# Kernel tuning notes

Hardware: AMD Instinct MI355X
Metric: run time of the kernel (lower is better)

## Reference

```python
import jax, jax.numpy as jnp
import numpy as np

D = 1024      # hidden_size
H = 16        # num_attention_heads
HD = D // H   # head_dim
FF = 4096     # intermediate_size
EPS = 1e-5

def layernorm(x, g, b):
    mu = jnp.mean(x, axis=-1, keepdims=True)
    var = jnp.mean(jnp.square(x - mu), axis=-1, keepdims=True)
    return (x - mu) * jax.lax.rsqrt(var + EPS) * g + b

def setup_inputs() -> dict:
    key = jax.random.key(0)
    ks = jax.random.split(key, 16)
    s = 0.02
    return {
        "x":   jax.random.normal(ks[0], (4, 1024, D), jnp.float32),
        "wq":  jax.random.normal(ks[1], (D, D), jnp.float32) * s,
        "bq":  jnp.zeros((D,), jnp.float32),
        "wk":  jax.random.normal(ks[2], (D, D), jnp.float32) * s,
        "bk":  jnp.zeros((D,), jnp.float32),
        "wv":  jax.random.normal(ks[3], (D, D), jnp.float32) * s,
        "bv":  jnp.zeros((D,), jnp.float32),
        "wo":  jax.random.normal(ks[4], (D, D), jnp.float32) * s,
        "bo":  jnp.zeros((D,), jnp.float32),
        "w1":  jax.random.normal(ks[5], (D, FF), jnp.float32) * s,
        "b1":  jnp.zeros((FF,), jnp.float32),
        "w2":  jax.random.normal(ks[6], (FF, D), jnp.float32) * s,
        "b2":  jnp.zeros((D,), jnp.float32),
        "ln1_g": jnp.ones((D,), jnp.float32),
        "ln1_b": jnp.zeros((D,), jnp.float32),
        "ln2_g": jnp.ones((D,), jnp.float32),
        "ln2_b": jnp.zeros((D,), jnp.float32),
    }

def reference(x, wq, bq, wk, bk, wv, bv, wo, bo, w1, b1, w2, b2,
              ln1_g, ln1_b, ln2_g, ln2_b):
    B, S, _ = x.shape
    # --- pre-LN multi-head attention (per-head linears fused as one GEMM) ---
    h = layernorm(x, ln1_g, ln1_b)
    q = (h @ wq + bq).reshape(B, S, H, HD).transpose(0, 2, 1, 3)  # [B,H,S,hd]
    k = (h @ wk + bk).reshape(B, S, H, HD).transpose(0, 2, 1, 3)
    v = (h @ wv + bv).reshape(B, S, H, HD).transpose(0, 2, 1, 3)
    scores = jnp.einsum('bhqd,bhkd->bhqk', q, k) / np.sqrt(HD).astype(x.dtype)
    weights = jax.nn.softmax(scores, axis=-1)  # dropout p=0 -> identity
    attn = jnp.einsum('bhqk,bhkd->bhqd', weights, v)
    attn = attn.transpose(0, 2, 1, 3).reshape(B, S, D)
    x = x + attn @ wo + bo
    # --- pre-LN feed-forward with exact GELU ---
    h2 = layernorm(x, ln2_g, ln2_b)
    ffn = jax.nn.gelu(h2 @ w1 + b1, approximate=False) @ w2 + b2
    return x + ffn
```

## Files before the change

kernel.cpp:

```cpp
#include <hip/hip_runtime.h>
#include <hip/hip_bf16.h>
#include <cstdint>

#define S_LEN  1024
#define DMODEL 1024
#define NTOK   4096
#define NHEAD  16
#define HDIM   64
#define FFDIM  4096
#define NBATCH 4
#define QSCALE 0.1803368801f

using bf16x8 = __attribute__((ext_vector_type(8))) short;
using f32x4  = __attribute__((ext_vector_type(4))) float;

__device__ __forceinline__ ushort f2bf(float f) {
  union { float f; uint32_t u; } a; a.f = f;
  uint32_t u = a.u;
  u += 0x7FFFu + ((u >> 16) & 1u);
  return (ushort)(u >> 16);
}
__device__ __forceinline__ ushort f2bf_hw(float f) {
  uint32_t r;
  asm("v_cvt_pk_bf16_f32 %0, %1, %1" : "=v"(r) : "v"(f));
  return (ushort)r;
}
__device__ __forceinline__ float bf2f(ushort u) {
  union { uint32_t u; float f; } c; c.u = ((uint32_t)u) << 16; return c.f;
}
__device__ __forceinline__ float ld_as_float(const float* p, long i) { return p[i]; }
__device__ __forceinline__ float ld_as_float(const ushort* p, long i) { return bf2f(p[i]); }
__device__ __forceinline__ void st_out(float* C, long i, float v) { C[i] = v; }
__device__ __forceinline__ void st_out(ushort* C, long i, float v) { C[i] = f2bf(v); }

__device__ __forceinline__ void gld_lds16(const void* g, void* l) {
  __builtin_amdgcn_global_load_lds((const __attribute__((address_space(1))) void*)g,
                                   (__attribute__((address_space(3))) void*)l, 16, 0, 0);
}

__global__ __launch_bounds__(256) void ln_kernel(const float* __restrict__ x,
    const float* __restrict__ g, const float* __restrict__ b,
    ushort* __restrict__ out) {
  int row = blockIdx.x;
  int tid = threadIdx.x;
  const float4* xr = (const float4*)(x + (long)row * DMODEL);
  float4 v = xr[tid];
  float s  = v.x + v.y + v.z + v.w;
  float s2 = v.x*v.x + v.y*v.y + v.z*v.z + v.w*v.w;
  for (int off = 32; off; off >>= 1) { s += __shfl_down(s, off); s2 += __shfl_down(s2, off); }
  __shared__ float red[8];
  int wid = tid >> 6, lane = tid & 63;
  if (lane == 0) { red[wid] = s; red[wid + 4] = s2; }
  __syncthreads();
  if (tid == 0) {
    red[0] = red[0] + red[1] + red[2] + red[3];
    red[4] = red[4] + red[5] + red[6] + red[7];
  }
  __syncthreads();
  float mu  = red[0] * (1.0f / DMODEL);
  float var = red[4] * (1.0f / DMODEL) - mu * mu;
  float rs  = rsqrtf(var + 1e-5f);
  float4 gg = ((const float4*)g)[tid];
  float4 bb = ((const float4*)b)[tid];
  ushort4 o;
  o.x = f2bf((v.x - mu) * rs * gg.x + bb.x);
  o.y = f2bf((v.y - mu) * rs * gg.y + bb.y);
  o.z = f2bf((v.z - mu) * rs * gg.z + bb.z);
  o.w = f2bf((v.w - mu) * rs * gg.w + bb.w);
  ((ushort4*)(out + (long)row * DMODEL))[tid] = o;
}

__global__ __launch_bounds__(256) void concat3(const float* __restrict__ a,
    const float* __restrict__ b, const float* __restrict__ c, float* __restrict__ o) {
  int i = blockIdx.x * 256 + threadIdx.x;
  o[i] = (i < 1024) ? a[i] : ((i < 2048) ? b[i - 1024] : c[i - 2048]);
}

template <int NP>
__global__ __launch_bounds__(256) void reduce_add(
    const ushort* __restrict__ parts, const float* __restrict__ bias,
    float* __restrict__ out) {
  long i = (long)blockIdx.x * 256 + threadIdx.x;
  const long PSTRIDE = (long)NTOK * DMODEL / 4;
  float4 acc = ((const float4*)out)[i];
  float4 b = ((const float4*)bias)[i & 255];
  acc.x += b.x; acc.y += b.y; acc.z += b.z; acc.w += b.w;
#pragma unroll
  for (int z = 0; z < NP; ++z) {
    ushort4 u = ((const ushort4*)parts)[z * PSTRIDE + i];
    acc.x += bf2f(u.x); acc.y += bf2f(u.y); acc.z += bf2f(u.z); acc.w += bf2f(u.w);
  }
  ((float4*)out)[i] = acc;
}

template <int NP>
__global__ __launch_bounds__(256) void reduce_ln(
    const ushort* __restrict__ parts, const float* __restrict__ xres,
    const float* __restrict__ bias, float* __restrict__ out,
    const float* __restrict__ g, const float* __restrict__ bln,
    ushort* __restrict__ hout) {
  int row = blockIdx.x, tid = threadIdx.x;
  long i = (long)row * 256 + tid;
  const long PSTRIDE = (long)NTOK * DMODEL / 4;
  float4 v = ((const float4*)xres)[i];
  float4 b = ((const float4*)bias)[tid];
  v.x += b.x; v.y += b.y; v.z += b.z; v.w += b.w;
#pragma unroll
  for (int z = 0; z < NP; ++z) {
    ushort4 u = ((const ushort4*)parts)[z * PSTRIDE + i];
    v.x += bf2f(u.x); v.y += bf2f(u.y); v.z += bf2f(u.z); v.w += bf2f(u.w);
  }
  ((float4*)out)[i] = v;
  float s  = v.x + v.y + v.z + v.w;
  float s2 = v.x*v.x + v.y*v.y + v.z*v.z + v.w*v.w;
  for (int off = 32; off; off >>= 1) { s += __shfl_down(s, off); s2 += __shfl_down(s2, off); }
  __shared__ float red[8];
  int wid = tid >> 6, lane = tid & 63;
  if (lane == 0) { red[wid] = s; red[wid + 4] = s2; }
  __syncthreads();
  if (tid == 0) {
    red[0] = red[0] + red[1] + red[2] + red[3];
    red[4] = red[4] + red[5] + red[6] + red[7];
  }
  __syncthreads();
  float mu  = red[0] * (1.0f / DMODEL);
  float var = red[4] * (1.0f / DMODEL) - mu * mu;
  float rs  = rsqrtf(var + 1e-5f);
  float4 gg = ((const float4*)g)[tid];
  float4 bb = ((const float4*)bln)[tid];
  ushort4 o;
  o.x = f2bf((v.x - mu) * rs * gg.x + bb.x);
  o.y = f2bf((v.y - mu) * rs * gg.y + bb.y);
  o.z = f2bf((v.z - mu) * rs * gg.z + bb.z);
  o.w = f2bf((v.w - mu) * rs * gg.w + bb.w);
  ((ushort4*)hout)[i] = o;
}

template <typename TIN>
__global__ __launch_bounds__(256) void transpose_cvt(const TIN* __restrict__ in,
    ushort* __restrict__ out, int ldin, int ldout,
    long inZhi, long inZlo, long outZ) {
  int z = blockIdx.z;
  in  += (long)(z >> 4) * inZhi + (long)(z & 15) * inZlo;
  out += (long)z * outZ;
  __shared__ float tile[32][33];
  int c0 = blockIdx.x * 32, r0 = blockIdx.y * 32;
  int tx = threadIdx.x, ty = threadIdx.y;
  for (int i = ty; i < 32; i += 8)
    tile[i][tx] = ld_as_float(in, (long)(r0 + i) * ldin + c0 + tx);
  __syncthreads();
  for (int i = ty; i < 32; i += 8)
    out[(long)(c0 + i) * ldout + r0 + tx] = f2bf(tile[tx][i]);
}

template <int ACT, bool BIAS, bool RES, typename TOUT>
__global__ __launch_bounds__(256) void gemm_bt(
    const ushort* __restrict__ A, const ushort* __restrict__ BT, TOUT* __restrict__ C,
    const float* __restrict__ bias, const float* __restrict__ resp,
    int M, int K, int lda, int ldb, int ldc,
    long aZhi, long aZlo, long bZhi, long bZlo, long cZhi, long cZlo) {
  __shared__ __align__(16) ushort lA[2][128 * 64];
  __shared__ __align__(16) ushort lB[2][128 * 64];
  int z = blockIdx.z;
  A  += (long)(z >> 4) * aZhi + (long)(z & 15) * aZlo;
  BT += (long)(z >> 4) * bZhi + (long)(z & 15) * bZlo;
  long coff = (long)(z >> 4) * cZhi + (long)(z & 15) * cZlo;
  int gx = gridDim.x;
  int nwg = gx * gridDim.y;
  int lin = blockIdx.x + gx * blockIdx.y;
  int wg = (lin & 7) * (nwg >> 3) + (lin >> 3);
  int n0 = (wg / gx) * 128, m0 = (wg % gx) * 128;
  int tid = threadIdx.x, lane = tid & 63, wid = tid >> 6;
  int wr = wid >> 1, wc = wid & 1;
  int lrow = lane >> 3;
  int swz = ((lane & 7) ^ lrow) << 3;
  int Mm1 = M - 1;
  f32x4 acc[4][4];
#pragma unroll
  for (int i = 0; i < 4; i++)
#pragma unroll
    for (int j = 0; j < 4; j++) acc[i][j] = (f32x4){0.f, 0.f, 0.f, 0.f};

  auto STAGE = [&](int kt, int buf) {
    const ushort* Ak = A + (kt << 6) + swz;
    const ushort* Bk = BT + (kt << 6) + swz;
#pragma unroll
    for (int c = 0; c < 4; ++c) {
      int ch = (wid << 2) | c;
      int rb = (ch << 3) + lrow;
      gld_lds16(Ak + (long)(n0 + rb) * lda, &lA[buf][ch << 9]);
      int mrow = min(m0 + rb, Mm1);
      gld_lds16(Bk + (long)mrow * ldb, &lB[buf][ch << 9]);
    }
  };

  int nK = K >> 6;
  STAGE(0, 0);
  for (int kt = 0; kt < nK; ++kt) {
    int cur = kt & 1;
    if (kt + 1 < nK) {
      STAGE(kt + 1, cur ^ 1);
      asm volatile("s_waitcnt vmcnt(8)" ::: "memory");
    } else {
      asm volatile("s_waitcnt vmcnt(0)" ::: "memory");
    }
    __builtin_amdgcn_s_barrier();
    __builtin_amdgcn_sched_barrier(0);
#pragma unroll
    for (int kk = 0; kk < 2; ++kk) {
      int g = (kk << 2) | (lane >> 4);
      int kfs = ((g ^ (lane & 7)) << 3);
      bf16x8 af[4], bfr[4];
#pragma unroll
      for (int i = 0; i < 4; i++) {
        af[i]  = *(const bf16x8*)(&lA[cur][((wr << 6) + (i << 4) + (lane & 15)) * 64 + kfs]);
        bfr[i] = *(const bf16x8*)(&lB[cur][((wc << 6) + (i << 4) + (lane & 15)) * 64 + kfs]);
      }
#pragma unroll
      for (int i = 0; i < 4; i++)
#pragma unroll
        for (int j = 0; j < 4; j++)
          acc[i][j] = __builtin_amdgcn_mfma_f32_16x16x32_bf16(af[i], bfr[j], acc[i][j], 0, 0, 0);
    }
    asm volatile("s_waitcnt lgkmcnt(0)" ::: "memory");
    __builtin_amdgcn_s_barrier();
    __builtin_amdgcn_sched_barrier(0);
  }
#pragma unroll
  for (int i = 0; i < 4; i++) {
    int rbase = n0 + wr * 64 + i * 16 + ((lane >> 4) << 2);
#pragma unroll
    for (int j = 0; j < 4; j++) {
      int col = m0 + wc * 64 + j * 16 + (lane & 15);
      if (col < M) {
        float bv = BIAS ? bias[col] : 0.0f;
#pragma unroll
        for (int q = 0; q < 4; q++) {
          int rowg = rbase + q;
          float vv = acc[i][j][q] + bv;
          if (ACT == 1) vv = 0.5f * vv * (1.0f + erff(vv * 0.70710678118f));
          long idx = coff + (long)rowg * ldc + col;
          if (RES) vv += resp[idx];
          st_out(C, idx, vv);
        }
      }
    }
  }
}

template <int ACT, bool BIAS, typename TOUT>
__global__ __launch_bounds__(512, 2) void gemm256(
    const ushort* __restrict__ A, const ushort* __restrict__ BT, TOUT* __restrict__ C,
    const float* __restrict__ bias,
    int K, int lda, int ldb, int ldc, long aZlo, long bZlo, long cZlo) {
  __shared__ __align__(16) ushort lA[2][256 * 64];
  __shared__ __align__(16) ushort lB[2][256 * 64];
  int z = blockIdx.z;
  A  += (long)z * aZlo;
  BT += (long)z * bZlo;
  C  += (long)z * cZlo;
  int gx = gridDim.x;
  int nwg = gx * gridDim.y;
  int lin = blockIdx.x + gx * blockIdx.y;
  int wg = (lin & 7) * (nwg >> 3) + (lin >> 3);
  int n0 = (wg / gx) * 256, m0 = (wg % gx) * 256;
  int tid = threadIdx.x, lane = tid & 63, wid = tid >> 6;
  int wm = wid >> 2, wn = wid & 3;
  int lo = lane & 15, hi = lane >> 4;
  int l7 = lane & 7;
  int srow = tid >> 3;
  int skg  = (tid & 7) ^ (srow & 7);
  const ushort* gA = A + (long)(n0 + srow) * lda + (skg << 3);
  const ushort* gB = BT + (long)(m0 + srow) * ldb + (skg << 3);

  f32x4 acc[8][4];
#pragma unroll
  for (int i = 0; i < 8; ++i)
#pragma unroll
    for (int j = 0; j < 4; ++j) acc[i][j] = (f32x4){0.f, 0.f, 0.f, 0.f};

  auto STG = [&](int kt, int buf, int c) {
    if (c < 4)
      gld_lds16(gA + (long)(c * 64) * lda + (kt << 6), &lA[buf][c * 4096 + wid * 512]);
    else
      gld_lds16(gB + (long)((c - 4) * 64) * ldb + (kt << 6), &lB[buf][(c - 4) * 4096 + wid * 512]);
  };

  int nK = K >> 6;
  STG(0, 0, 4); STG(0, 0, 5); STG(0, 0, 6); STG(0, 0, 7);
  STG(0, 0, 0); STG(0, 0, 1); STG(0, 0, 2); STG(0, 0, 3);
  STG(1, 1, 4); STG(1, 1, 5); STG(1, 1, 6); STG(1, 1, 7);
  asm volatile("s_waitcnt vmcnt(4)" ::: "memory");
  __builtin_amdgcn_s_barrier();

  for (int t = 0; t < nK; ++t) {
    int cur = t & 1, nxt = cur ^ 1;
    ushort* plA = &lA[cur][0];
    ushort* plB = &lB[cur][0];
    bf16x8 bfr[4][2];
#pragma unroll
    for (int p = 0; p < 4; ++p) {
      if (p == 0) {
#pragma unroll
        for (int j = 0; j < 4; ++j)
#pragma unroll
          for (int kk = 0; kk < 2; ++kk)
            bfr[j][kk] = *(const bf16x8*)&plB[(wn * 64 + j * 16 + lo) * 64 +
                                             ((((kk << 2) | hi) ^ l7) << 3)];
      }
      bf16x8 afr[2][2];
#pragma unroll
      for (int ii = 0; ii < 2; ++ii)
#pragma unroll
        for (int kk = 0; kk < 2; ++kk)
          afr[ii][kk] = *(const bf16x8*)&plA[(wm * 128 + (p * 2 + ii) * 16 + lo) * 64 +
                                             ((((kk << 2) | hi) ^ l7) << 3)];
      if (p == 0 && t + 1 < nK) { STG(t + 1, nxt, 0); STG(t + 1, nxt, 1); }
      if (p == 1 && t + 1 < nK) { STG(t + 1, nxt, 2); STG(t + 1, nxt, 3); }
      if (p == 2 && t + 2 < nK) { STG(t + 2, cur, 4); STG(t + 2, cur, 5); }
      if (p == 3 && t + 2 < nK) { STG(t + 2, cur, 6); STG(t + 2, cur, 7); }
      __builtin_amdgcn_s_barrier();
      asm volatile("s_waitcnt lgkmcnt(0)" ::: "memory");
      __builtin_amdgcn_sched_barrier(0);
      __builtin_amdgcn_s_setprio(1);
#pragma unroll
      for (int ii = 0; ii < 2; ++ii)
#pragma unroll
        for (int j = 0; j < 4; ++j)
#pragma unroll
          for (int kk = 0; kk < 2; ++kk)
            acc[p * 2 + ii][j] = __builtin_amdgcn_mfma_f32_16x16x32_bf16(
                afr[ii][kk], bfr[j][kk], acc[p * 2 + ii][j], 0, 0, 0);
      __builtin_amdgcn_s_setprio(0);
      __builtin_amdgcn_sched_barrier(0);
      if (p == 3 && t + 1 < nK) {
        if (t + 2 < nK) asm volatile("s_waitcnt vmcnt(4)" ::: "memory");
        else            asm volatile("s_waitcnt vmcnt(0)" ::: "memory");
      }
      __builtin_amdgcn_s_barrier();
    }
  }

#pragma unroll
  for (int i = 0; i < 8; ++i) {
    int rbase = n0 + wm * 128 + i * 16 + hi * 4;
#pragma unroll
    for (int j = 0; j < 4; ++j) {
      int colg = m0 + wn * 64 + j * 16 + lo;
      float bv = BIAS ? bias[colg] : 0.0f;
#pragma unroll
      for (int q = 0; q < 4; ++q) {
        float vv = acc[i][j][q] + bv;
        if (ACT == 1) vv = 0.5f * vv * (1.0f + erff(vv * 0.70710678118f));
        if (ACT == 2 && colg < DMODEL) vv *= QSCALE;
        long idx = (long)(rbase + q) * ldc + colg;
        st_out(C, idx, vv);
      }
    }
  }
}

#define QBLK 64
#define KBLK 128
__global__ __launch_bounds__(256) void flash_attn(
    const ushort* __restrict__ qkv, const ushort* __restrict__ vt,
    ushort* __restrict__ attn) {
  __shared__ __align__(16) ushort lK[2][KBLK * 64];
  __shared__ __align__(16) ushort lV[2][64 * KBLK];
  __shared__ __align__(16) ushort lP[4 * 16 * KBLK];

  int qt = blockIdx.x, bh = blockIdx.z;
  int b = bh >> 4, hh = bh & 15;
  int tid = threadIdx.x, lane = tid & 63, wid = tid >> 6;
  int lo = lane & 15, hi = lane >> 4;
  int lrow = lane >> 3;
  int swz8 = ((lane & 7) ^ lrow) << 3;

  const ushort* Qg = qkv + (long)(b * 1024 + qt * QBLK) * 3072 + hh * 64;
  const ushort* Kg = qkv + (long)(b * 1024) * 3072 + 1024 + hh * 64;
  const ushort* Vg = vt + (long)bh * 64 * 1024;
  ushort* lPw = lP + wid * (16 * KBLK);

  bf16x8 kOnes;
#pragma unroll
  for (int i = 0; i < 8; ++i) kOnes[i] = (short)0x3F80;

  auto STAGE = [&](int t, int buf) {
#pragma unroll
    for (int c = 0; c < 4; ++c) {
      int ch = (wid << 2) | c;
      int rb = (ch << 3) + lrow;
      gld_lds16(Kg + (long)(t * KBLK + rb) * 3072 + swz8, &lK[buf][ch << 9]);
    }
#pragma unroll
    for (int c = 0; c < 4; ++c) {
      int ch = (wid << 2) | c;
      int hd = (ch << 2) + hi;
      gld_lds16(Vg + (long)hd * 1024 + t * KBLK + ((lo ^ (hd & 7)) << 3), &lV[buf][ch << 9]);
    }
  };

#pragma unroll
  for (int c = 0; c < 2; ++c) {
    int ch = wid * 2 + c;
    int rb = ch * 8 + lrow;
    gld_lds16(Qg + (long)rb * 3072 + swz8, &lP[ch << 9]);
  }
  STAGE(0, 0);
  asm volatile("s_waitcnt vmcnt(8)" ::: "memory");
  __builtin_amdgcn_sched_barrier(0);
  bf16x8 a_q[2];
#pragma unroll
  for (int kk = 0; kk < 2; ++kk)
    a_q[kk] = *(const bf16x8*)&lP[(wid * 16 + lo) * 64 + (((kk * 4 + hi) ^ (lo & 7)) << 3)];
  asm volatile("s_waitcnt lgkmcnt(0)" ::: "memory");
  __builtin_amdgcn_sched_barrier(0);
  __builtin_amdgcn_s_barrier();

  float m_run[4];
#pragma unroll
  for (int q = 0; q < 4; ++q) m_run[q] = -1e30f;
  f32x4 acc_o[4];
#pragma unroll
  for (int j = 0; j < 4; ++j) acc_o[j] = (f32x4){0.f, 0.f, 0.f, 0.f};
  f32x4 acc_l = (f32x4){0.f, 0.f, 0.f, 0.f};

  for (int t = 0; t < 8; ++t) {
    int cur = t & 1;
    if (t + 1 < 8) {
      STAGE(t + 1, cur ^ 1);
      asm volatile("s_waitcnt vmcnt(8)" ::: "memory");
    } else {
      asm volatile("s_waitcnt vmcnt(0)" ::: "memory");
    }
    __builtin_amdgcn_s_barrier();
    __builtin_amdgcn_sched_barrier(0);

    f32x4 s[8];
#pragma unroll
    for (int j = 0; j < 8; ++j) s[j] = (f32x4){0.f, 0.f, 0.f, 0.f};
    __builtin_amdgcn_s_setprio(1);
#pragma unroll
    for (int kk = 0; kk < 2; ++kk) {
      int slot = ((kk * 4 + hi) ^ (lo & 7)) << 3;
#pragma unroll
      for (int j = 0; j < 8; ++j) {
        bf16x8 bk = *(const bf16x8*)&lK[cur][(j * 16 + lo) * 64 + slot];
        s[j] = __builtin_amdgcn_mfma_f32_16x16x32_bf16(a_q[kk], bk, s[j], 0, 0, 0);
      }
    }
    __builtin_amdgcn_s_setprio(0);

    float alpha[4];
#pragma unroll
    for (int q = 0; q < 4; ++q) {
      float m = fmaxf(fmaxf(fmaxf(s[0][q], s[1][q]), fmaxf(s[2][q], s[3][q])),
                      fmaxf(fmaxf(s[4][q], s[5][q]), fmaxf(s[6][q], s[7][q])));
#pragma unroll
      for (int off = 1; off < 16; off <<= 1) m = fmaxf(m, __shfl_xor(m, off));
      float mnew = fmaxf(m_run[q], m);
      alpha[q] = __builtin_amdgcn_exp2f(m_run[q] - mnew);
      m_run[q] = mnew;
    }
#pragma unroll
    for (int j = 0; j < 8; ++j)
#pragma unroll
      for (int q = 0; q < 4; ++q) {
        float e = __builtin_amdgcn_exp2f(s[j][q] - m_run[q]);
        int row = hi * 4 + q;
        int col = j * 16 + lo;
        lPw[row * KBLK + (col ^ ((row & 7) << 3))] = f2bf_hw(e);
      }

#pragma unroll
    for (int q = 0; q < 4; ++q) acc_l[q] *= alpha[q];
#pragma unroll
    for (int j = 0; j < 4; ++j)
#pragma unroll
      for (int q = 0; q < 4; ++q) acc_o[j][q] *= alpha[q];
    __builtin_amdgcn_s_setprio(1);
#pragma unroll
    for (int ks = 0; ks < 4; ++ks) {
      int slot = ((ks * 4 + hi) ^ (lo & 7)) << 3;
      bf16x8 ap = *(const bf16x8*)&lPw[lo * KBLK + slot];
      acc_l = __builtin_amdgcn_mfma_f32_16x16x32_bf16(ap, kOnes, acc_l, 0, 0, 0);
#pragma unroll
      for (int j = 0; j < 4; ++j) {
        bf16x8 bv = *(const bf16x8*)&lV[cur][(j * 16 + lo) * KBLK + slot];
        acc_o[j] = __builtin_amdgcn_mfma_f32_16x16x32_bf16(ap, bv, acc_o[j], 0, 0, 0);
      }
    }
    __builtin_amdgcn_s_setprio(0);
    asm volatile("s_waitcnt lgkmcnt(0)" ::: "memory");
    __builtin_amdgcn_s_barrier();
    __builtin_amdgcn_sched_barrier(0);
  }

#pragma unroll
  for (int q = 0; q < 4; ++q) {
    float linv = 1.0f / acc_l[q];
    int qrow = qt * QBLK + wid * 16 + hi * 4 + q;
#pragma unroll
    for (int j = 0; j < 4; ++j)
      attn[(long)(b * 1024 + qrow) * 1024 + hh * 64 + j * 16 + lo] = f2bf(acc_o[j][q] * linv);
  }
}

extern "C" void kernel_launch(void* const* d_in, const int* in_sizes, int n_in,
                              void* d_out, int out_size, void* d_ws, size_t ws_size,
                              hipStream_t stream) {
  const float* x    = (const float*)d_in[0];
  const float* wq   = (const float*)d_in[1];
  const float* bq   = (const float*)d_in[2];
  const float* wk   = (const float*)d_in[3];
  const float* bk   = (const float*)d_in[4];
  const float* wv   = (const float*)d_in[5];
  const float* bv   = (const float*)d_in[6];
  const float* wo   = (const float*)d_in[7];
  const float* bo   = (const float*)d_in[8];
  const float* w1   = (const float*)d_in[9];
  const float* b1   = (const float*)d_in[10];
  const float* w2   = (const float*)d_in[11];
  const float* b2   = (const float*)d_in[12];
  const float* ln1g = (const float*)d_in[13];
  const float* ln1b = (const float*)d_in[14];
  const float* ln2g = (const float*)d_in[15];
  const float* ln2b = (const float*)d_in[16];
  float* out = (float*)d_out;

  char* ws = (char*)d_ws;
  size_t off = 0;
  auto alloc = [&](size_t bytes) { void* p = ws + off; off += (bytes + 255) & ~(size_t)255; return p; };
  ushort* h     = (ushort*)alloc((size_t)NTOK * DMODEL * 2);
  ushort* wqkvT = (ushort*)alloc((size_t)3 * DMODEL * DMODEL * 2);
  ushort* woT   = (ushort*)alloc((size_t)DMODEL * DMODEL * 2);
  float*  bqkv  = (float*)alloc((size_t)3 * DMODEL * 4);
  ushort* qkv   = (ushort*)alloc((size_t)NTOK * 3 * DMODEL * 2);
  ushort* vt    = (ushort*)alloc((size_t)64 * HDIM * S_LEN * 2);
  ushort* attn  = (ushort*)alloc((size_t)NTOK * DMODEL * 2);
  ushort* w1T   = (ushort*)alloc((size_t)DMODEL * FFDIM * 2);
  ushort* w2T   = (ushort*)alloc((size_t)FFDIM * DMODEL * 2);
  ushort* gact  = (ushort*)alloc((size_t)NTOK * FFDIM * 2);
  ushort* woPart  = qkv;
  ushort* ffnPart = qkv;

  dim3 tb32(32, 8);
  hipLaunchKernelGGL((transpose_cvt<float>), dim3(DMODEL/32, DMODEL/32, 1), tb32, 0, stream,
                     wq, wqkvT, DMODEL, DMODEL, 0, 0, 0);
  hipLaunchKernelGGL((transpose_cvt<float>), dim3(DMODEL/32, DMODEL/32, 1), tb32, 0, stream,
                     wk, wqkvT + (size_t)DMODEL * DMODEL, DMODEL, DMODEL, 0, 0, 0);
  hipLaunchKernelGGL((transpose_cvt<float>), dim3(DMODEL/32, DMODEL/32, 1), tb32, 0, stream,
                     wv, wqkvT + (size_t)2 * DMODEL * DMODEL, DMODEL, DMODEL, 0, 0, 0);
  hipLaunchKernelGGL((transpose_cvt<float>), dim3(DMODEL/32, DMODEL/32, 1), tb32, 0, stream,
                     wo, woT, DMODEL, DMODEL, 0, 0, 0);
  hipLaunchKernelGGL(concat3, dim3(12), dim3(256), 0, stream, bq, bk, bv, bqkv);

  hipLaunchKernelGGL(ln_kernel, dim3(NTOK), dim3(256), 0, stream, x, ln1g, ln1b, h);

  hipLaunchKernelGGL((gemm256<2, true, ushort>), dim3(12, 16, 1), dim3(512), 0, stream,
                     h, wqkvT, qkv, bqkv, DMODEL, DMODEL, DMODEL, 3 * DMODEL, 0L, 0L, 0L);

  hipLaunchKernelGGL((transpose_cvt<ushort>), dim3(HDIM/32, S_LEN/32, 64), tb32, 0, stream,
                     qkv + 2 * DMODEL, vt, 3 * DMODEL, S_LEN,
                     (long)S_LEN * 3 * DMODEL, 64L, (long)HDIM * S_LEN);

  hipLaunchKernelGGL(flash_attn, dim3(16, 1, 64), dim3(256), 0, stream, qkv, vt, attn);

  hipLaunchKernelGGL((gemm_bt<0, false, false, ushort>), dim3(8, 32, 2), dim3(256), 0, stream,
                     attn, woT, woPart, (const float*)nullptr, (const float*)nullptr,
                     DMODEL, 512, DMODEL, DMODEL, DMODEL,
                     0L, 512L, 0L, 512L, 0L, (long)NTOK * DMODEL);
  hipLaunchKernelGGL((reduce_ln<2>), dim3(4096), dim3(256), 0, stream,
                     woPart, x, bo, out, ln2g, ln2b, h);
  hipLaunchKernelGGL((transpose_cvt<float>), dim3(FFDIM/32, DMODEL/32, 1), tb32, 0, stream,
                     w1, w1T, FFDIM, DMODEL, 0, 0, 0);
  hipLaunchKernelGGL((transpose_cvt<float>), dim3(DMODEL/32, FFDIM/32, 1), tb32, 0, stream,
                     w2, w2T, DMODEL, FFDIM, 0, 0, 0);
  hipLaunchKernelGGL((gemm256<1, true, ushort>), dim3(16, 16, 1), dim3(512), 0, stream,
                     h, w1T, gact, b1, DMODEL, DMODEL, DMODEL, FFDIM, 0L, 0L, 0L);
  hipLaunchKernelGGL((gemm256<0, false, ushort>), dim3(4, 16, 4), dim3(512), 0, stream,
                     gact, w2T, ffnPart, (const float*)nullptr,
                     1024, FFDIM, FFDIM, DMODEL, 1024L, 1024L, (long)NTOK * DMODEL);
  hipLaunchKernelGGL((reduce_add<4>), dim3(4096), dim3(256), 0, stream,
                     ffnPart, b2, out);
  (void)in_sizes; (void)n_in; (void)out_size; (void)ws_size;
}
```

Measured before the change: 252.9 us.

## Restructure GEMM k-loop to double-buffer A fragments and cut barriers

```diff
diff --git a/kernel.cpp b/kernel.cpp
--- a/kernel.cpp
+++ b/kernel.cpp
@@ -298,31 +298,17 @@
     ushort* plA = &lA[cur][0];
     ushort* plB = &lB[cur][0];
     bf16x8 bfr[4][2];
-#pragma unroll
-    for (int p = 0; p < 4; ++p) {
-      if (p == 0) {
-#pragma unroll
-        for (int j = 0; j < 4; ++j)
-#pragma unroll
-          for (int kk = 0; kk < 2; ++kk)
-            bfr[j][kk] = *(const bf16x8*)&plB[(wn * 64 + j * 16 + lo) * 64 +
-                                             ((((kk << 2) | hi) ^ l7) << 3)];
-      }
-      bf16x8 afr[2][2];
+    bf16x8 afrA[2][2], afrB[2][2];
+
+    auto RDA = [&](bf16x8 (&a)[2][2], int p) {
 #pragma unroll
       for (int ii = 0; ii < 2; ++ii)
 #pragma unroll
         for (int kk = 0; kk < 2; ++kk)
-          afr[ii][kk] = *(const bf16x8*)&plA[(wm * 128 + (p * 2 + ii) * 16 + lo) * 64 +
-                                             ((((kk << 2) | hi) ^ l7) << 3)];
-      if (p == 0 && t + 1 < nK) { STG(t + 1, nxt, 0); STG(t + 1, nxt, 1); }
-      if (p == 1 && t + 1 < nK) { STG(t + 1, nxt, 2); STG(t + 1, nxt, 3); }
-      if (p == 2 && t + 2 < nK) { STG(t + 2, cur, 4); STG(t + 2, cur, 5); }
-      if (p == 3 && t + 2 < nK) { STG(t + 2, cur, 6); STG(t + 2, cur, 7); }
-      __builtin_amdgcn_s_barrier();
-      asm volatile("s_waitcnt lgkmcnt(0)" ::: "memory");
-      __builtin_amdgcn_sched_barrier(0);
-      __builtin_amdgcn_s_setprio(1);
+          a[ii][kk] = *(const bf16x8*)&plA[(wm * 128 + (p * 2 + ii) * 16 + lo) * 64 +
+                                           ((((kk << 2) | hi) ^ l7) << 3)];
+    };
+    auto MF = [&](bf16x8 (&a)[2][2], int p) {
 #pragma unroll
       for (int ii = 0; ii < 2; ++ii)
 #pragma unroll
@@ -330,15 +316,38 @@
 #pragma unroll
           for (int kk = 0; kk < 2; ++kk)
             acc[p * 2 + ii][j] = __builtin_amdgcn_mfma_f32_16x16x32_bf16(
-                afr[ii][kk], bfr[j][kk], acc[p * 2 + ii][j], 0, 0, 0);
-      __builtin_amdgcn_s_setprio(0);
-      __builtin_amdgcn_sched_barrier(0);
-      if (p == 3 && t + 1 < nK) {
-        if (t + 2 < nK) asm volatile("s_waitcnt vmcnt(4)" ::: "memory");
-        else            asm volatile("s_waitcnt vmcnt(0)" ::: "memory");
-      }
-      __builtin_amdgcn_s_barrier();
-    }
+                a[ii][kk], bfr[j][kk], acc[p * 2 + ii][j], 0, 0, 0);
+    };
+
+#pragma unroll
+    for (int j = 0; j < 4; ++j)
+#pragma unroll
+      for (int kk = 0; kk < 2; ++kk)
+        bfr[j][kk] = *(const bf16x8*)&plB[(wn * 64 + j * 16 + lo) * 64 +
+                                          ((((kk << 2) | hi) ^ l7) << 3)];
+    RDA(afrA, 0);
+    RDA(afrB, 1);
+    if (t + 1 < nK) { STG(t + 1, nxt, 0); STG(t + 1, nxt, 1); STG(t + 1, nxt, 2); STG(t + 1, nxt, 3); }
+    asm volatile("s_waitcnt lgkmcnt(0)" ::: "memory");
+    __builtin_amdgcn_sched_barrier(0);
+    __builtin_amdgcn_s_barrier();
+    __builtin_amdgcn_sched_barrier(0);
+    if (t + 2 < nK) { STG(t + 2, cur, 4); STG(t + 2, cur, 5); STG(t + 2, cur, 6); STG(t + 2, cur, 7); }
+
+    __builtin_amdgcn_s_setprio(1);
+    MF(afrA, 0);
+    RDA(afrA, 2);
+    MF(afrB, 1);
+    RDA(afrB, 3);
+    MF(afrA, 2);
+    MF(afrB, 3);
+    __builtin_amdgcn_s_setprio(0);
+    __builtin_amdgcn_sched_barrier(0);
+    if (t + 1 < nK) {
+      if (t + 2 < nK) asm volatile("s_waitcnt vmcnt(4)" ::: "memory");
+      else            asm volatile("s_waitcnt vmcnt(0)" ::: "memory");
+    }
+    __builtin_amdgcn_s_barrier();
   }
 
 #pragma unroll
```

Result: slower. 259.5 us (+2.6%).
